# Performance work log

Measured on AMD Instinct MI355X. Metric: run time of the kernel, lower is better.

## Reference

```python
import jax, jax.numpy as jnp
import numpy as np

N = 100000       # num_nodes
E = 1600000      # num_edges (avg degree 16)
EL = 200000      # link-prediction edges
IN_C = 64
POS = 16
HID = 64
OUT = 32


def setup_inputs() -> dict:
    key = jax.random.key(0)
    ks = jax.random.split(key, 10)
    def glorot(k, shape):
        scale = 1.0 / np.sqrt(shape[0])
        return jax.random.uniform(k, shape, jnp.float32, -scale, scale)
    return {
        "x": jax.random.normal(ks[0], (N, IN_C), jnp.float32),
        "pos_emb": jax.random.normal(ks[1], (N, POS), jnp.float32),
        "W1": glorot(ks[2], (IN_C + POS, HID)),
        "b1": jnp.zeros((HID,), jnp.float32),
        "W2": glorot(ks[3], (HID, OUT)),
        "b2": jnp.zeros((OUT,), jnp.float32),
        "Wl": glorot(ks[4], (2 * OUT, 1)),
        "bl": jnp.zeros((1,), jnp.float32),
        "edge_index": jax.random.randint(ks[5], (2, E), 0, N, jnp.int32),
        "edge_label_index": jax.random.randint(ks[6], (2, EL), 0, N, jnp.int32),
    }


def reference(x, pos_emb, W1, b1, W2, b2, Wl, bl, edge_index, edge_label_index):
    n = x.shape[0]
    # GCNConv: add self-loops, symmetric deg^{-1/2} normalization (PyG defaults)
    loops = jnp.arange(n, dtype=edge_index.dtype)
    src = jnp.concatenate([edge_index[0], loops])  # [E+N]
    dst = jnp.concatenate([edge_index[1], loops])  # [E+N]
    deg = jax.ops.segment_sum(jnp.ones_like(dst, jnp.float32), dst, num_segments=n)
    dinv = jnp.where(deg > 0, jax.lax.rsqrt(jnp.maximum(deg, 1e-12)), 0.0)
    norm = dinv[src] * dinv[dst]  # [E+N]

    def gcn_conv(h, W, b):
        hw = h @ W                                    # [N, d_out] transform first
        msg = hw[src] * norm[:, None]                 # gather + normalize
        return jax.ops.segment_sum(msg, dst, num_segments=n) + b  # scatter-add

    h = jnp.concatenate([x, pos_emb], axis=1)         # [N, in+pos]
    h = jax.nn.relu(gcn_conv(h, W1, b1))              # dropout is eval no-op
    z = gcn_conv(h, W2, b2)                           # [N, out]

    s, d = edge_label_index[0], edge_label_index[1]
    zc = jnp.concatenate([z[s], z[d]], axis=1)        # [EL, 2*out]
    edge_pred = (zc @ Wl + bl)[:, 0]                  # [EL]
    return z, edge_pred
```

## Files before the change

### kernel.cpp

```cpp
#include <hip/hip_runtime.h>
#include <hip/hip_fp16.h>

#define NN 100000
#define NE 1600000
#define NEL 200000
#define TM 64
#define TM2 128

#define NBUCK 196
#define CAPB  10240
#define TPE   8192

__global__ __launch_bounds__(256) void k_part(const int* __restrict__ src,
                                              const int* __restrict__ dst,
                                              int* __restrict__ gcur,
                                              int* __restrict__ part) {
    __shared__ int hist[NBUCK];
    __shared__ int base[NBUCK];
    __shared__ int rk[NBUCK];
    int tid = threadIdx.x;
    for (int i = tid; i < NBUCK; i += 256) { hist[i] = 0; rk[i] = 0; }
    __syncthreads();
    int e0 = blockIdx.x * TPE;
    int e1 = min(e0 + TPE, NE);
    for (int e = e0 + tid; e < e1; e += 256)
        atomicAdd(&hist[dst[e] >> 9], 1);
    __syncthreads();
    for (int i = tid; i < NBUCK; i += 256)
        base[i] = i * CAPB + atomicAdd(&gcur[i], hist[i]);
    __syncthreads();
    for (int e = e0 + tid; e < e1; e += 256) {
        int d = dst[e];
        int s = src[e];
        int b = d >> 9;
        int r = atomicAdd(&rk[b], 1);
        part[base[b] + r] = ((d & 511) << 17) | s;
    }
}

__global__ __launch_bounds__(256) void k_build(const int* __restrict__ gcur,
                                               const int* __restrict__ part,
                                               int* __restrict__ csr,
                                               int* __restrict__ off,
                                               float* __restrict__ dinv) {
    __shared__ int cnts[256];
    __shared__ int hist[512];
    __shared__ int loff[512];
    __shared__ int ssum[256];
    __shared__ int csrbuf[CAPB];
    int b = blockIdx.x;
    int tid = threadIdx.x;
    cnts[tid] = (tid < NBUCK) ? gcur[tid] : 0;
    __syncthreads();
    for (int st = 1; st < 256; st <<= 1) {
        int tmp = (tid >= st) ? cnts[tid - st] : 0;
        __syncthreads();
        cnts[tid] += tmp;
        __syncthreads();
    }
    int obase = (b == 0) ? 0 : cnts[b - 1];
    int cnt = gcur[b];
    int pbase = b * CAPB;
    hist[tid] = 0; hist[tid + 256] = 0;
    __syncthreads();
    for (int i = tid; i < cnt; i += 256)
        atomicAdd(&hist[part[pbase + i] >> 17], 1);
    __syncthreads();
    int a0 = hist[2 * tid], a1 = hist[2 * tid + 1];
    int pairs = a0 + a1;
    ssum[tid] = pairs;
    __syncthreads();
    for (int st = 1; st < 256; st <<= 1) {
        int tmp = (tid >= st) ? ssum[tid - st] : 0;
        __syncthreads();
        ssum[tid] += tmp;
        __syncthreads();
    }
    int pexcl = ssum[tid] - pairs;
    loff[2 * tid] = pexcl;
    loff[2 * tid + 1] = pexcl + a0;
    __syncthreads();
    for (int i = tid; i < 512; i += 256) {
        int d = b * 512 + i;
        if (d < NN) {
            int c = hist[i];
            off[d] = obase + loff[i] + c;
            dinv[d] = rsqrtf((float)(c + 1));
        }
    }
    hist[tid] = 0; hist[tid + 256] = 0;
    __syncthreads();
    for (int i = tid; i < cnt; i += 256) {
        int rec = part[pbase + i];
        int dl = rec >> 17;
        int r = atomicAdd(&hist[dl], 1);
        csrbuf[loff[dl] + r] = rec & 0x1FFFF;
    }
    __syncthreads();
    for (int i = tid; i < cnt; i += 256)
        csr[obase + i] = csrbuf[i];
}

__global__ __launch_bounds__(256) void k_hw1(const float* __restrict__ x,
                                             const float* __restrict__ pos,
                                             const float* __restrict__ W1,
                                             const float* __restrict__ dinv,
                                             __half* __restrict__ hw1) {
    __shared__ float sh[TM * 80];
    __shared__ float sw[80 * 64];
    int tid = threadIdx.x;
    for (int t = tid; t < 80 * 64; t += 256) sw[t] = W1[t];
    int nb = blockIdx.x * TM;
    for (int i = tid; i < TM * 64; i += 256) {
        int node = i >> 6, ch = i & 63;
        int g = nb + node;
        sh[node * 80 + ch] = (g < NN) ? x[g * 64 + ch] : 0.0f;
    }
    for (int i = tid; i < TM * 16; i += 256) {
        int node = i >> 4, ch = i & 15;
        int g = nb + node;
        sh[node * 80 + 64 + ch] = (g < NN) ? pos[g * 16 + ch] : 0.0f;
    }
    __syncthreads();
    int j  = (tid & 15) * 4;
    int nl = (tid >> 4) * 4;
    float a00=0,a01=0,a02=0,a03=0, a10=0,a11=0,a12=0,a13=0;
    float a20=0,a21=0,a22=0,a23=0, a30=0,a31=0,a32=0,a33=0;
#pragma unroll 4
    for (int k = 0; k < 80; ++k) {
        float4 wv = *(const float4*)&sw[k * 64 + j];
        float h0 = sh[(nl + 0) * 80 + k];
        float h1 = sh[(nl + 1) * 80 + k];
        float h2 = sh[(nl + 2) * 80 + k];
        float h3 = sh[(nl + 3) * 80 + k];
        a00 += h0 * wv.x; a01 += h0 * wv.y; a02 += h0 * wv.z; a03 += h0 * wv.w;
        a10 += h1 * wv.x; a11 += h1 * wv.y; a12 += h1 * wv.z; a13 += h1 * wv.w;
        a20 += h2 * wv.x; a21 += h2 * wv.y; a22 += h2 * wv.z; a23 += h2 * wv.w;
        a30 += h3 * wv.x; a31 += h3 * wv.y; a32 += h3 * wv.z; a33 += h3 * wv.w;
    }
    int g0 = nb + nl;
    union { __half2 h2v[2]; float2 f2; } u;
#define STORE_ROW(r, b0, b1, b2, b3)                                          \
    if (g0 + r < NN) {                                                        \
        float sc = dinv[g0 + r];                                              \
        u.h2v[0] = __floats2half2_rn(b0 * sc, b1 * sc);                       \
        u.h2v[1] = __floats2half2_rn(b2 * sc, b3 * sc);                       \
        *(float2*)&hw1[(g0 + r) * 64 + j] = u.f2;                             \
    }
    STORE_ROW(0, a00, a01, a02, a03)
    STORE_ROW(1, a10, a11, a12, a13)
    STORE_ROW(2, a20, a21, a22, a23)
    STORE_ROW(3, a30, a31, a32, a33)
#undef STORE_ROW
}

__global__ __launch_bounds__(256) void k_gather1(const int* __restrict__ off,
                                                 const int* __restrict__ csr,
                                                 const float* __restrict__ dinv,
                                                 const __half* __restrict__ hw,
                                                 const float* __restrict__ b1,
                                                 __half* __restrict__ h2out) {
    int lane = threadIdx.x & 63;
    int wave = threadIdx.x >> 6;
    int d = blockIdx.x * 4 + wave;
    int start = (d == 0) ? 0 : off[d - 1];
    int end = off[d];
    start = __builtin_amdgcn_readfirstlane(start);
    end   = __builtin_amdgcn_readfirstlane(end);
    float dd = dinv[d];
    float hself = __half2float(hw[d * 64 + lane]);
    float acc0 = 0.0f, acc1 = 0.0f, acc2 = 0.0f, acc3 = 0.0f;
    int e = start;
    for (; e + 7 < end; e += 8) {
        int s0 = csr[e],     s1 = csr[e + 1];
        int s2 = csr[e + 2], s3 = csr[e + 3];
        int s4 = csr[e + 4], s5 = csr[e + 5];
        int s6 = csr[e + 6], s7 = csr[e + 7];
        float g0 = __half2float(hw[s0 * 64 + lane]);
        float g1 = __half2float(hw[s1 * 64 + lane]);
        float g2 = __half2float(hw[s2 * 64 + lane]);
        float g3 = __half2float(hw[s3 * 64 + lane]);
        float g4 = __half2float(hw[s4 * 64 + lane]);
        float g5 = __half2float(hw[s5 * 64 + lane]);
        float g6 = __half2float(hw[s6 * 64 + lane]);
        float g7 = __half2float(hw[s7 * 64 + lane]);
        acc0 += g0; acc1 += g1; acc2 += g2; acc3 += g3;
        acc0 += g4; acc1 += g5; acc2 += g6; acc3 += g7;
    }
    for (; e < end; ++e)
        acc0 += __half2float(hw[csr[e] * 64 + lane]);
    float v = fmaxf(b1[lane] + dd * (((acc0 + acc1) + (acc2 + acc3)) + hself), 0.0f);
    h2out[d * 64 + lane] = __float2half_rn(v);
}

__global__ __launch_bounds__(256) void k_hw2(const __half* __restrict__ h2,
                                             const float* __restrict__ W2,
                                             const float* __restrict__ dinv,
                                             __half* __restrict__ hw2) {
    __shared__ float sh[TM2 * 65];
    __shared__ float sw[64 * 32];
    int tid = threadIdx.x;
    for (int t = tid; t < 64 * 32; t += 256) sw[t] = W2[t];
    int nb = blockIdx.x * TM2;
    for (int i = tid; i < TM2 * 64; i += 256) {
        int node = i >> 6, ch = i & 63;
        int g = nb + node;
        sh[node * 65 + ch] = (g < NN) ? __half2float(h2[g * 64 + ch]) : 0.0f;
    }
    __syncthreads();
    int j  = (tid & 7) * 4;
    int nl = (tid >> 3) * 4;
    float a00=0,a01=0,a02=0,a03=0, a10=0,a11=0,a12=0,a13=0;
    float a20=0,a21=0,a22=0,a23=0, a30=0,a31=0,a32=0,a33=0;
#pragma unroll 4
    for (int k = 0; k < 64; ++k) {
        float4 wv = *(const float4*)&sw[k * 32 + j];
        float h0 = sh[(nl + 0) * 65 + k];
        float h1 = sh[(nl + 1) * 65 + k];
        float h2v = sh[(nl + 2) * 65 + k];
        float h3 = sh[(nl + 3) * 65 + k];
        a00 += h0 * wv.x;  a01 += h0 * wv.y;  a02 += h0 * wv.z;  a03 += h0 * wv.w;
        a10 += h1 * wv.x;  a11 += h1 * wv.y;  a12 += h1 * wv.z;  a13 += h1 * wv.w;
        a20 += h2v * wv.x; a21 += h2v * wv.y; a22 += h2v * wv.z; a23 += h2v * wv.w;
        a30 += h3 * wv.x;  a31 += h3 * wv.y;  a32 += h3 * wv.z;  a33 += h3 * wv.w;
    }
    int g0 = nb + nl;
    union { __half2 h2v2[2]; float2 f2; } u;
#define STORE_ROW(r, b0, b1, b2, b3)                                          \
    if (g0 + r < NN) {                                                        \
        float sc = dinv[g0 + r];                                              \
        u.h2v2[0] = __floats2half2_rn(b0 * sc, b1 * sc);                      \
        u.h2v2[1] = __floats2half2_rn(b2 * sc, b3 * sc);                      \
        *(float2*)&hw2[(g0 + r) * 32 + j] = u.f2;                             \
    }
    STORE_ROW(0, a00, a01, a02, a03)
    STORE_ROW(1, a10, a11, a12, a13)
    STORE_ROW(2, a20, a21, a22, a23)
    STORE_ROW(3, a30, a31, a32, a33)
#undef STORE_ROW
}

__global__ __launch_bounds__(256) void k_gather2(const int* __restrict__ off,
                                                 const int* __restrict__ csr,
                                                 const float* __restrict__ dinv,
                                                 const __half* __restrict__ hw,
                                                 const float* __restrict__ b2,
                                                 float* __restrict__ outz) {
    int lane = threadIdx.x & 63;
    int half = lane >> 5;
    int j = lane & 31;
    int wave = threadIdx.x >> 6;
    int d = blockIdx.x * 4 + wave;
    int start = (d == 0) ? 0 : off[d - 1];
    int end = off[d];
    start = __builtin_amdgcn_readfirstlane(start);
    end   = __builtin_amdgcn_readfirstlane(end);
    float dd = dinv[d];
    float hself = __half2float(hw[d * 32 + j]);
    float accA = 0.0f, accB = 0.0f, accC = 0.0f, accD = 0.0f;
    int e = start;
    for (; e + 7 < end; e += 8) {
        int sA = csr[e + half];
        int sB = csr[e + half + 2];
        int sC = csr[e + half + 4];
        int sD = csr[e + half + 6];
        accA += __half2float(hw[sA * 32 + j]);
        accB += __half2float(hw[sB * 32 + j]);
        accC += __half2float(hw[sC * 32 + j]);
        accD += __half2float(hw[sD * 32 + j]);
    }
    for (int ee = e + half; ee < end; ee += 2)
        accA += __half2float(hw[csr[ee] * 32 + j]);
    float acc = (accA + accB) + (accC + accD);
    acc += __shfl(acc, lane ^ 32, 64);
    if (half == 0)
        outz[d * 32 + j] = b2[j] + dd * (acc + hself);
}

__global__ __launch_bounds__(256) void k_linkpred(const int* __restrict__ sidx,
                                                  const int* __restrict__ didx,
                                                  const float* __restrict__ z,
                                                  const float* __restrict__ Wl,
                                                  const float* __restrict__ bl,
                                                  float* __restrict__ pred) {
    int t = blockIdx.x * blockDim.x + threadIdx.x;
    int e = t >> 4;
    int l = t & 15;
    int s = sidx[e], d = didx[e];
    float2 zs = *(const float2*)&z[s * 32 + 2 * l];
    float2 zd = *(const float2*)&z[d * 32 + 2 * l];
    float2 ws = *(const float2*)&Wl[2 * l];
    float2 wd = *(const float2*)&Wl[32 + 2 * l];
    float v = zs.x * ws.x + zs.y * ws.y + zd.x * wd.x + zd.y * wd.y;
    v += __shfl_xor(v, 1, 64);
    v += __shfl_xor(v, 2, 64);
    v += __shfl_xor(v, 4, 64);
    v += __shfl_xor(v, 8, 64);
    if (l == 0) pred[e] = v + bl[0];
}

extern "C" void kernel_launch(void* const* d_in, const int* in_sizes, int n_in,
                              void* d_out, int out_size, void* d_ws, size_t ws_size,
                              hipStream_t stream) {
    const float* x    = (const float*)d_in[0];
    const float* pos  = (const float*)d_in[1];
    const float* W1   = (const float*)d_in[2];
    const float* b1   = (const float*)d_in[3];
    const float* W2   = (const float*)d_in[4];
    const float* b2   = (const float*)d_in[5];
    const float* Wl   = (const float*)d_in[6];
    const float* bl   = (const float*)d_in[7];
    const int*   ei   = (const int*)d_in[8];
    const int*   eli  = (const int*)d_in[9];
    const int* src  = ei;
    const int* dst  = ei + NE;
    const int* lsrc = eli;
    const int* ldst = eli + NEL;

    float* out_z    = (float*)d_out;
    float* out_pred = (float*)d_out + NN * 32;

    float*  dinv  = (float*)d_ws;
    int*    off   = (int*)(dinv + NN);
    int*    gcur  = off + NN;
    int*    csr   = gcur + NBUCK;
    __half* hw1   = (__half*)(csr + NE);
    int*    part  = (int*)hw1;
    __half* h2    = hw1 + NN * 64;
    __half* hw2   = h2 + NN * 64;

    hipMemsetAsync(gcur, 0, NBUCK * sizeof(int), stream);
    k_part<<<(NE + TPE - 1) / TPE, 256, 0, stream>>>(src, dst, gcur, part);
    k_build<<<NBUCK, 256, 0, stream>>>(gcur, part, csr, off, dinv);

    k_hw1<<<(NN + TM - 1) / TM, 256, 0, stream>>>(x, pos, W1, dinv, hw1);

    k_gather1<<<NN / 4, 256, 0, stream>>>(off, csr, dinv, hw1, b1, h2);

    k_hw2<<<(NN + TM2 - 1) / TM2, 256, 0, stream>>>(h2, W2, dinv, hw2);

    k_gather2<<<NN / 4, 256, 0, stream>>>(off, csr, dinv, hw2, b2, out_z);

    k_linkpred<<<NEL * 16 / 256, 256, 0, stream>>>(lsrc, ldst, out_z, Wl, bl, out_pred);
}
```

Before: 310.8 us.

## Vectorize neighbor gathers and precompute per-node link-prediction projections

Rewrites both GCN gather kernels so each lane loads four half channels per edge and several edges are processed in parallel across lane groups, reduced by cross-lane shuffles. The second gather also computes per-node dot products of z with both halves of the link weight, so link prediction becomes two scalar gathers per edge instead of two full z-row gathers. This targets memory-instruction count and gather traffic. In exchange, the edge-index loads read past each node's range (masked), and some lanes do wasted work on low-degree nodes.

```diff
diff --git a/kernel.cpp b/kernel.cpp
--- a/kernel.cpp
+++ b/kernel.cpp
@@ -161,6 +161,8 @@
                                                  const float* __restrict__ b1,
                                                  __half* __restrict__ h2out) {
     int lane = threadIdx.x & 63;
+    int q  = lane >> 4;
+    int cl = lane & 15;
     int wave = threadIdx.x >> 6;
     int d = blockIdx.x * 4 + wave;
     int start = (d == 0) ? 0 : off[d - 1];
@@ -168,29 +170,58 @@
     start = __builtin_amdgcn_readfirstlane(start);
     end   = __builtin_amdgcn_readfirstlane(end);
     float dd = dinv[d];
-    float hself = __half2float(hw[d * 64 + lane]);
-    float acc0 = 0.0f, acc1 = 0.0f, acc2 = 0.0f, acc3 = 0.0f;
-    int e = start;
-    for (; e + 7 < end; e += 8) {
-        int s0 = csr[e],     s1 = csr[e + 1];
-        int s2 = csr[e + 2], s3 = csr[e + 3];
-        int s4 = csr[e + 4], s5 = csr[e + 5];
-        int s6 = csr[e + 6], s7 = csr[e + 7];
-        float g0 = __half2float(hw[s0 * 64 + lane]);
-        float g1 = __half2float(hw[s1 * 64 + lane]);
-        float g2 = __half2float(hw[s2 * 64 + lane]);
-        float g3 = __half2float(hw[s3 * 64 + lane]);
-        float g4 = __half2float(hw[s4 * 64 + lane]);
-        float g5 = __half2float(hw[s5 * 64 + lane]);
-        float g6 = __half2float(hw[s6 * 64 + lane]);
-        float g7 = __half2float(hw[s7 * 64 + lane]);
-        acc0 += g0; acc1 += g1; acc2 += g2; acc3 += g3;
-        acc0 += g4; acc1 += g5; acc2 += g6; acc3 += g7;
-    }
-    for (; e < end; ++e)
-        acc0 += __half2float(hw[csr[e] * 64 + lane]);
-    float v = fmaxf(b1[lane] + dd * (((acc0 + acc1) + (acc2 + acc3)) + hself), 0.0f);
-    h2out[d * 64 + lane] = __float2half_rn(v);
+    uint2 selfbits = *(const uint2*)&hw[d * 64 + 4 * cl];
+    float4 acc = make_float4(0.f, 0.f, 0.f, 0.f);
+    for (int e = start; e < end; e += 32) {
+        int sv[32];
+#pragma unroll
+        for (int j = 0; j < 32; ++j) sv[j] = csr[e + j];
+        int srow[8]; float msk[8];
+#pragma unroll
+        for (int k = 0; k < 8; ++k) {
+            int s01 = (q & 1) ? sv[4 * k + 1] : sv[4 * k + 0];
+            int s23 = (q & 1) ? sv[4 * k + 3] : sv[4 * k + 2];
+            int s   = (q & 2) ? s23 : s01;
+            int rem = end - e - 4 * k;
+            bool valid = q < rem;
+            srow[k] = valid ? s : d;
+            msk[k]  = valid ? 1.0f : 0.0f;
+        }
+        uint2 g[8];
+#pragma unroll
+        for (int k = 0; k < 8; ++k)
+            g[k] = *(const uint2*)&hw[srow[k] * 64 + 4 * cl];
+#pragma unroll
+        for (int k = 0; k < 8; ++k) {
+            float2 lo = __half22float2(*(__half2*)&g[k].x);
+            float2 hi = __half22float2(*(__half2*)&g[k].y);
+            acc.x = fmaf(msk[k], lo.x, acc.x);
+            acc.y = fmaf(msk[k], lo.y, acc.y);
+            acc.z = fmaf(msk[k], hi.x, acc.z);
+            acc.w = fmaf(msk[k], hi.y, acc.w);
+        }
+    }
+    acc.x += __shfl_xor(acc.x, 16, 64);
+    acc.y += __shfl_xor(acc.y, 16, 64);
+    acc.z += __shfl_xor(acc.z, 16, 64);
+    acc.w += __shfl_xor(acc.w, 16, 64);
+    acc.x += __shfl_xor(acc.x, 32, 64);
+    acc.y += __shfl_xor(acc.y, 32, 64);
+    acc.z += __shfl_xor(acc.z, 32, 64);
+    acc.w += __shfl_xor(acc.w, 32, 64);
+    if (q == 0) {
+        float2 slo = __half22float2(*(__half2*)&selfbits.x);
+        float2 shi = __half22float2(*(__half2*)&selfbits.y);
+        float4 bv = *(const float4*)&b1[4 * cl];
+        float v0 = fmaxf(bv.x + dd * (acc.x + slo.x), 0.0f);
+        float v1 = fmaxf(bv.y + dd * (acc.y + slo.y), 0.0f);
+        float v2 = fmaxf(bv.z + dd * (acc.z + shi.x), 0.0f);
+        float v3 = fmaxf(bv.w + dd * (acc.w + shi.y), 0.0f);
+        union { __half2 h[2]; float2 f; } u;
+        u.h[0] = __floats2half2_rn(v0, v1);
+        u.h[1] = __floats2half2_rn(v2, v3);
+        *(float2*)&h2out[d * 64 + 4 * cl] = u.f;
+    }
 }
 
 __global__ __launch_bounds__(256) void k_hw2(const __half* __restrict__ h2,
@@ -231,7 +262,7 @@
         float sc = dinv[g0 + r];                                              \
         u.h2v2[0] = __floats2half2_rn(b0 * sc, b1 * sc);                      \
         u.h2v2[1] = __floats2half2_rn(b2 * sc, b3 * sc);                      \
-        *(float2*)&hw2[(g0 + r) * 32 + j] = u.f2;                             \
+        *(float2*)&hw2[(g0 + r) * 32 + j] = u.f2;                            \
     }
     STORE_ROW(0, a00, a01, a02, a03)
     STORE_ROW(1, a10, a11, a12, a13)
@@ -245,10 +276,13 @@
                                                  const float* __restrict__ dinv,
                                                  const __half* __restrict__ hw,
                                                  const float* __restrict__ b2,
-                                                 float* __restrict__ outz) {
+                                                 const float* __restrict__ Wl,
+                                                 float* __restrict__ outz,
+                                                 float* __restrict__ uu,
+                                                 float* __restrict__ vv) {
     int lane = threadIdx.x & 63;
-    int half = lane >> 5;
-    int j = lane & 31;
+    int g8 = lane >> 3;
+    int cl = lane & 7;
     int wave = threadIdx.x >> 6;
     int d = blockIdx.x * 4 + wave;
     int start = (d == 0) ? 0 : off[d - 1];
@@ -256,47 +290,78 @@
     start = __builtin_amdgcn_readfirstlane(start);
     end   = __builtin_amdgcn_readfirstlane(end);
     float dd = dinv[d];
-    float hself = __half2float(hw[d * 32 + j]);
-    float accA = 0.0f, accB = 0.0f, accC = 0.0f, accD = 0.0f;
-    int e = start;
-    for (; e + 7 < end; e += 8) {
-        int sA = csr[e + half];
-        int sB = csr[e + half + 2];
-        int sC = csr[e + half + 4];
-        int sD = csr[e + half + 6];
-        accA += __half2float(hw[sA * 32 + j]);
-        accB += __half2float(hw[sB * 32 + j]);
-        accC += __half2float(hw[sC * 32 + j]);
-        accD += __half2float(hw[sD * 32 + j]);
-    }
-    for (int ee = e + half; ee < end; ee += 2)
-        accA += __half2float(hw[csr[ee] * 32 + j]);
-    float acc = (accA + accB) + (accC + accD);
-    acc += __shfl(acc, lane ^ 32, 64);
-    if (half == 0)
-        outz[d * 32 + j] = b2[j] + dd * (acc + hself);
+    uint2 selfbits = *(const uint2*)&hw[d * 32 + 4 * cl];
+    float4 acc = make_float4(0.f, 0.f, 0.f, 0.f);
+    for (int e = start; e < end; e += 32) {
+        int sv[32];
+#pragma unroll
+        for (int j = 0; j < 32; ++j) sv[j] = csr[e + j];
+        int srow[4]; float msk[4];
+#pragma unroll
+        for (int k = 0; k < 4; ++k) {
+            int t0 = (g8 & 1) ? sv[8 * k + 1] : sv[8 * k + 0];
+            int t1 = (g8 & 1) ? sv[8 * k + 3] : sv[8 * k + 2];
+            int t2 = (g8 & 1) ? sv[8 * k + 5] : sv[8 * k + 4];
+            int t3 = (g8 & 1) ? sv[8 * k + 7] : sv[8 * k + 6];
+            int u0 = (g8 & 2) ? t1 : t0;
+            int u1 = (g8 & 2) ? t3 : t2;
+            int s  = (g8 & 4) ? u1 : u0;
+            int rem = end - e - 8 * k;
+            bool valid = g8 < rem;
+            srow[k] = valid ? s : d;
+            msk[k]  = valid ? 1.0f : 0.0f;
+        }
+        uint2 g[4];
+#pragma unroll
+        for (int k = 0; k < 4; ++k)
+            g[k] = *(const uint2*)&hw[srow[k] * 32 + 4 * cl];
+#pragma unroll
+        for (int k = 0; k < 4; ++k) {
+            float2 lo = __half22float2(*(__half2*)&g[k].x);
+            float2 hi = __half22float2(*(__half2*)&g[k].y);
+            acc.x = fmaf(msk[k], lo.x, acc.x);
+            acc.y = fmaf(msk[k], lo.y, acc.y);
+            acc.z = fmaf(msk[k], hi.x, acc.z);
+            acc.w = fmaf(msk[k], hi.y, acc.w);
+        }
+    }
+#pragma unroll
+    for (int m = 8; m <= 32; m <<= 1) {
+        acc.x += __shfl_xor(acc.x, m, 64);
+        acc.y += __shfl_xor(acc.y, m, 64);
+        acc.z += __shfl_xor(acc.z, m, 64);
+        acc.w += __shfl_xor(acc.w, m, 64);
+    }
+    if (g8 == 0) {
+        float2 slo = __half22float2(*(__half2*)&selfbits.x);
+        float2 shi = __half22float2(*(__half2*)&selfbits.y);
+        float4 bv = *(const float4*)&b2[4 * cl];
+        float4 z;
+        z.x = bv.x + dd * (acc.x + slo.x);
+        z.y = bv.y + dd * (acc.y + slo.y);
+        z.z = bv.z + dd * (acc.z + shi.x);
+        z.w = bv.w + dd * (acc.w + shi.y);
+        *(float4*)&outz[d * 32 + 4 * cl] = z;
+        float4 ws = *(const float4*)&Wl[4 * cl];
+        float4 wd = *(const float4*)&Wl[32 + 4 * cl];
+        float p0 = z.x * ws.x + z.y * ws.y + z.z * ws.z + z.w * ws.w;
+        float p1 = z.x * wd.x + z.y * wd.y + z.z * wd.z + z.w * wd.w;
+        p0 += __shfl_xor(p0, 1, 64); p1 += __shfl_xor(p1, 1, 64);
+        p0 += __shfl_xor(p0, 2, 64); p1 += __shfl_xor(p1, 2, 64);
+        p0 += __shfl_xor(p0, 4, 64); p1 += __shfl_xor(p1, 4, 64);
+        if (cl == 0) { uu[d] = p0; vv[d] = p1; }
+    }
 }
 
 __global__ __launch_bounds__(256) void k_linkpred(const int* __restrict__ sidx,
                                                   const int* __restrict__ didx,
-                                                  const float* __restrict__ z,
-                                                  const float* __restrict__ Wl,
+                                                  const float* __restrict__ uu,
+                                                  const float* __restrict__ vv,
                                                   const float* __restrict__ bl,
                                                   float* __restrict__ pred) {
-    int t = blockIdx.x * blockDim.x + threadIdx.x;
-    int e = t >> 4;
-    int l = t & 15;
-    int s = sidx[e], d = didx[e];
-    float2 zs = *(const float2*)&z[s * 32 + 2 * l];
-    float2 zd = *(const float2*)&z[d * 32 + 2 * l];
-    float2 ws = *(const float2*)&Wl[2 * l];
-    float2 wd = *(const float2*)&Wl[32 + 2 * l];
-    float v = zs.x * ws.x + zs.y * ws.y + zd.x * wd.x + zd.y * wd.y;
-    v += __shfl_xor(v, 1, 64);
-    v += __shfl_xor(v, 2, 64);
-    v += __shfl_xor(v, 4, 64);
-    v += __shfl_xor(v, 8, 64);
-    if (l == 0) pred[e] = v + bl[0];
+    int e = blockIdx.x * 256 + threadIdx.x;
+    if (e < NEL)
+        pred[e] = uu[sidx[e]] + vv[didx[e]] + bl[0];
 }
 
 extern "C" void kernel_launch(void* const* d_in, const int* in_sizes, int n_in,
@@ -328,6 +393,8 @@
     int*    part  = (int*)hw1;
     __half* h2    = hw1 + NN * 64;
     __half* hw2   = h2 + NN * 64;
+    float*  uu    = (float*)h2;
+    float*  vv    = uu + NN;
 
     hipMemsetAsync(gcur, 0, NBUCK * sizeof(int), stream);
     k_part<<<(NE + TPE - 1) / TPE, 256, 0, stream>>>(src, dst, gcur, part);
@@ -339,7 +406,9 @@
 
     k_hw2<<<(NN + TM2 - 1) / TM2, 256, 0, stream>>>(h2, W2, dinv, hw2);
 
-    k_gather2<<<NN / 4, 256, 0, stream>>>(off, csr, dinv, hw2, b2, out_z);
-
-    k_linkpred<<<NEL * 16 / 256, 256, 0, stream>>>(lsrc, ldst, out_z, Wl, bl, out_pred);
-}
+    k_gather2<<<NN / 4, 256, 0, stream>>>(off, csr, dinv, hw2, b2, Wl,
+                                          out_z, uu, vv);
+
+    k_linkpred<<<(NEL + 255) / 256, 256, 0, stream>>>(lsrc, ldst, uu, vv, bl,
+                                                      out_pred);
+}
```

Result: slower. 629.0 us (+102.4%).
